# Kernel tuning notes

Hardware: AMD Instinct MI355X
Metric: run time of the kernel (lower is better)

Reference implementation:

```python
import jax, jax.numpy as jnp
import numpy as np

N, E, IN, HID, H, L, G = 20000, 320000, 128, 64, 4, 3, 128

def setup_inputs() -> dict:
    key = jax.random.key(0)
    ks = jax.random.split(key, 14)
    x = jax.random.normal(ks[0], (N, IN), dtype=jnp.float32)
    edge_index = jax.random.randint(ks[1], (2, E), 0, N, dtype=jnp.int64)
    batch = jnp.sort(jax.random.randint(ks[2], (N,), 0, G, dtype=jnp.int64))
    s_in = 1.0 / np.sqrt(IN)
    s_h = 1.0 / np.sqrt(HID)
    lin_W = jax.random.normal(ks[3], (IN, HID), jnp.float32) * s_in
    lin_b = jax.random.normal(ks[4], (HID,), jnp.float32) * 0.02
    Wq = jax.random.normal(ks[5], (L, HID, H * HID), jnp.float32) * s_h
    bq = jax.random.normal(ks[6], (L, H * HID), jnp.float32) * 0.02
    Wk = jax.random.normal(ks[7], (L, HID, H * HID), jnp.float32) * s_h
    bk = jax.random.normal(ks[8], (L, H * HID), jnp.float32) * 0.02
    Wv = jax.random.normal(ks[9], (L, HID, H * HID), jnp.float32) * s_h
    bv = jax.random.normal(ks[10], (L, H * HID), jnp.float32) * 0.02
    Ws = jax.random.normal(ks[11], (L, HID, HID), jnp.float32) * s_h
    bs = jax.random.normal(ks[12], (L, HID), jnp.float32) * 0.02
    return {"x": x, "edge_index": edge_index, "batch": batch,
            "lin_W": lin_W, "lin_b": lin_b, "Wq": Wq, "bq": bq,
            "Wk": Wk, "bk": bk, "Wv": Wv, "bv": bv, "Ws": Ws, "bs": bs}

def _transformer_conv(h, src, dst, Wq, bq, Wk, bk, Wv, bv, Ws, bs):
    # PyG TransformerConv(hid, hid, heads=H, concat=False), beta=False, root_weight=True
    n = h.shape[0]
    C = HID  # per-head dim
    q = (h @ Wq + bq).reshape(n, H, C)
    k = (h @ Wk + bk).reshape(n, H, C)
    v = (h @ Wv + bv).reshape(n, H, C)
    # per-edge attention logits: q_i . k_j / sqrt(C), i=dst (target), j=src
    alpha = jnp.einsum('ehc,ehc->eh', q[dst], k[src]) * (1.0 / np.sqrt(C))  # [E,H]
    # segment softmax over edges grouped by target node
    amax = jax.ops.segment_max(alpha, dst, num_segments=n)  # [N,H]
    amax = jnp.where(jnp.isfinite(amax), amax, 0.0)
    ex = jnp.exp(alpha - amax[dst])
    denom = jax.ops.segment_sum(ex, dst, num_segments=n)
    a = ex / jnp.maximum(denom[dst], 1e-16)  # [E,H]
    msg = a[:, :, None] * v[src]  # [E,H,C]
    agg = jax.ops.segment_sum(msg.reshape(-1, H * C), dst, num_segments=n)
    out = agg.reshape(n, H, C).mean(axis=1)  # concat=False -> head mean
    return out + h @ Ws + bs  # root/skip connection

def reference(x, edge_index, batch, lin_W, lin_b, Wq, bq, Wk, bk, Wv, bv, Ws, bs):
    src, dst = edge_index[0], edge_index[1]
    h = x @ lin_W + lin_b  # [N, HID]; dropout inactive in eval
    for l in range(L):
        h = jax.nn.relu(_transformer_conv(h, src, dst, Wq[l], bq[l], Wk[l], bk[l],
                                          Wv[l], bv[l], Ws[l], bs[l]))
    # global_add_pool: sum node features per graph
    return jax.ops.segment_sum(h, batch, num_segments=G)  # [G, HID]
```

## Files before the change

kernel.cpp:

```cpp
#include <hip/hip_runtime.h>
#include <math.h>

#define N_NODES 20000
#define N_EDGES 320000
#define DIM_IN 128
#define HID 64
#define HEADS 4
#define LAYERS 3
#define GRAPHS 128
#define QSS 320

typedef unsigned short ushort;
typedef ushort ushort8 __attribute__((ext_vector_type(8)));
typedef short short8 __attribute__((ext_vector_type(8)));
typedef float f32x4 __attribute__((ext_vector_type(4)));

__device__ __forceinline__ float bf2f(ushort u) {
    return __uint_as_float(((unsigned int)u) << 16);
}
__device__ __forceinline__ ushort f2bf(float f) {
    unsigned int b = __float_as_uint(f);
    return (ushort)((b + 0x7FFFu + ((b >> 16) & 1u)) >> 16);
}


__global__ void hist_kernel(const int* __restrict__ dst, int* __restrict__ counts, int n) {
    int e = blockIdx.x * 256 + threadIdx.x;
    if (e < n) atomicAdd(&counts[dst[e]], 1);
}

__global__ __launch_bounds__(256) void blocksum_kernel(const int* __restrict__ counts,
                                                       int* __restrict__ bsum, int n) {
    int i = blockIdx.x * 256 + threadIdx.x;
    int v = (i < n) ? counts[i] : 0;
    int lane = threadIdx.x & 63, wave = threadIdx.x >> 6;
#pragma unroll
    for (int off = 32; off >= 1; off >>= 1) v += __shfl_xor(v, off);
    __shared__ int ws[4];
    if (lane == 0) ws[wave] = v;
    __syncthreads();
    if (threadIdx.x == 0) bsum[blockIdx.x] = ws[0] + ws[1] + ws[2] + ws[3];
}

__global__ __launch_bounds__(128) void scanb_kernel(const int* __restrict__ bsum,
                                                    int* __restrict__ bexcl, int nb) {
    int tid = threadIdx.x;
    int v = (tid < nb) ? bsum[tid] : 0;
    int lane = tid & 63, wave = tid >> 6;
    int s = v;
#pragma unroll
    for (int off = 1; off < 64; off <<= 1) {
        int t = __shfl_up(s, off);
        if (lane >= off) s += t;
    }
    __shared__ int w0sum;
    if (tid == 63) w0sum = s;
    __syncthreads();
    int excl = s - v + (wave ? w0sum : 0);
    if (tid < nb) bexcl[tid] = excl;
}

__global__ __launch_bounds__(256) void expand_kernel(const int* __restrict__ counts,
                                                     const int* __restrict__ bexcl,
                                                     int* __restrict__ offs,
                                                     int* __restrict__ cursor, int n) {
    int i = blockIdx.x * 256 + threadIdx.x;
    int v = (i < n) ? counts[i] : 0;
    int lane = threadIdx.x & 63, wave = threadIdx.x >> 6;
    int s = v;
#pragma unroll
    for (int off = 1; off < 64; off <<= 1) {
        int t = __shfl_up(s, off);
        if (lane >= off) s += t;
    }
    __shared__ int wsum[4];
    if (lane == 63) wsum[wave] = s;
    __syncthreads();
    int add = bexcl[blockIdx.x];
    for (int w = 0; w < wave; ++w) add += wsum[w];
    int excl = add + s - v;
    if (i < n) { offs[i] = excl; cursor[i] = excl; }
    if (i == 0) offs[n] = N_EDGES;
}

__global__ void scatter_kernel(const int* __restrict__ src, const int* __restrict__ dst,
                               int* __restrict__ cursor, int* __restrict__ csr, int n) {
    int e = blockIdx.x * 256 + threadIdx.x;
    if (e < n) {
        int d = dst[e];
        int pos = atomicAdd(&cursor[d], 1);
        csr[pos] = src[e];
    }
}


__global__ __launch_bounds__(256) void wcvt_all_kernel(
        const float* __restrict__ Wq, const float* __restrict__ bq,
        const float* __restrict__ Wk, const float* __restrict__ bk,
        const float* __restrict__ Wv, const float* __restrict__ bv,
        const float* __restrict__ Ws, const float* __restrict__ bs,
        const float* __restrict__ linW,
        ushort* __restrict__ Wt3, float* __restrict__ bias3,
        ushort* __restrict__ Wlt) {
    const int PER = 832 * 64;
    int idx = blockIdx.x * 256 + threadIdx.x;
    if (idx < 3 * PER) {
        int l = idx / PER;
        int r = idx - l * PER;
        int j = r >> 6, k = r & 63;
        const float* Wq_l = Wq + (size_t)l * HID * 256;
        const float* Wk_l = Wk + (size_t)l * HID * 256;
        const float* Wv_l = Wv + (size_t)l * HID * 256;
        const float* Ws_l = Ws + (size_t)l * HID * 64;
        float w;
        if (j < 256) {
            w = Wq_l[(size_t)k * 256 + j];
        } else if (j < 768) {
            int pout = j - 256;
            int isv = (pout >> 2) & 1;
            int low2 = pout & 3;
            int g = pout >> 3;
            int srccol = (g >> 4) * 64 + (g & 15) * 4 + low2;
            w = isv ? Wv_l[(size_t)k * 256 + srccol] : Wk_l[(size_t)k * 256 + srccol];
        } else {
            w = Ws_l[(size_t)k * 64 + (j - 768)];
        }
        Wt3[idx] = f2bf(w);
    } else {
        int idx2 = idx - 3 * PER;
        if (idx2 < 64 * DIM_IN) {
            int col = idx2 >> 7, k = idx2 & 127;
            Wlt[idx2] = f2bf(linW[(size_t)k * HID + col]);
        }
    }
    if (idx < 3 * 832) {
        int l = idx / 832, j = idx - l * 832;
        float b;
        if (j < 256) {
            b = bq[l * 256 + j];
        } else if (j < 768) {
            int pout = j - 256;
            int isv = (pout >> 2) & 1;
            int low2 = pout & 3;
            int g = pout >> 3;
            int srccol = (g >> 4) * 64 + (g & 15) * 4 + low2;
            b = isv ? bv[l * 256 + srccol] : bk[l * 256 + srccol];
        } else {
            b = bs[l * 64 + (j - 768)];
        }
        bias3[idx] = b;
    }
}


__global__ __launch_bounds__(256) void lin_kernel(const float* __restrict__ x,
                                                  const ushort* __restrict__ Wlt,
                                                  const float* __restrict__ lb,
                                                  float* __restrict__ h0) {
    int tid = threadIdx.x;
    int w = tid >> 6, l = tid & 63;
    int r0 = blockIdx.x * 64 + w * 16;
    int row = r0 + (l & 15);
    int rowc = (row < N_NODES) ? row : (N_NODES - 1);

    short8 a[4];
#pragma unroll
    for (int kc = 0; kc < 4; ++kc) {
        const float* xp = x + (size_t)rowc * DIM_IN + kc * 32 + (l >> 4) * 8;
        float4 f0 = *(const float4*)xp;
        float4 f1 = *(const float4*)(xp + 4);
        ushort8 u;
        u[0] = f2bf(f0.x); u[1] = f2bf(f0.y); u[2] = f2bf(f0.z); u[3] = f2bf(f0.w);
        u[4] = f2bf(f1.x); u[5] = f2bf(f1.y); u[6] = f2bf(f1.z); u[7] = f2bf(f1.w);
        a[kc] = __builtin_bit_cast(short8, u);
    }

    f32x4 acc[4];
#pragma unroll
    for (int t = 0; t < 4; ++t) acc[t] = (f32x4){0.f, 0.f, 0.f, 0.f};

    const ushort* wb = Wlt + (size_t)(l & 15) * DIM_IN + (l >> 4) * 8;
#pragma unroll
    for (int t = 0; t < 4; ++t) {
#pragma unroll
        for (int kc = 0; kc < 4; ++kc) {
            short8 b = *(const short8*)(wb + (size_t)t * 16 * DIM_IN + kc * 32);
            acc[t] = __builtin_amdgcn_mfma_f32_16x16x32_bf16(a[kc], b, acc[t], 0, 0, 0);
        }
    }

    int rbase = r0 + ((l >> 4) << 2);
#pragma unroll
    for (int t = 0; t < 4; ++t) {
        int col = t * 16 + (l & 15);
        float bias = lb[col];
#pragma unroll
        for (int i = 0; i < 4; ++i) {
            int rr = rbase + i;
            if (rr < N_NODES) h0[(size_t)rr * HID + col] = acc[t][i] + bias;
        }
    }
}


__global__ __launch_bounds__(512) void proj_kernel(const float* __restrict__ h,
                                                   const ushort* __restrict__ Wt,
                                                   const float* __restrict__ bias_cat,
                                                   float* __restrict__ qs,
                                                   ushort* __restrict__ kvpack) {
    int tid = threadIdx.x;
    int w = tid >> 6, l = tid & 63;
    int r0 = blockIdx.x * 32 + (w & 1) * 16;
    int c0 = (w >> 1) * 208;
    int row = r0 + (l & 15);
    int koff = (l >> 4) * 8;

    short8 a[2];
#pragma unroll
    for (int m = 0; m < 2; ++m) {
        const float* hp = h + (size_t)row * HID + m * 32 + koff;
        float4 f0 = *(const float4*)hp;
        float4 f1 = *(const float4*)(hp + 4);
        ushort8 u;
        u[0] = f2bf(f0.x); u[1] = f2bf(f0.y); u[2] = f2bf(f0.z); u[3] = f2bf(f0.w);
        u[4] = f2bf(f1.x); u[5] = f2bf(f1.y); u[6] = f2bf(f1.z); u[7] = f2bf(f1.w);
        a[m] = __builtin_bit_cast(short8, u);
    }

    f32x4 acc[13];
#pragma unroll
    for (int t = 0; t < 13; ++t) acc[t] = (f32x4){0.f, 0.f, 0.f, 0.f};

    const ushort* wb = Wt + ((size_t)(c0 + (l & 15))) * HID + koff;
#pragma unroll
    for (int t = 0; t < 13; ++t) {
        short8 b0 = *(const short8*)(wb + (size_t)t * 16 * HID);
        short8 b1 = *(const short8*)(wb + (size_t)t * 16 * HID + 32);
        acc[t] = __builtin_amdgcn_mfma_f32_16x16x32_bf16(a[0], b0, acc[t], 0, 0, 0);
        acc[t] = __builtin_amdgcn_mfma_f32_16x16x32_bf16(a[1], b1, acc[t], 0, 0, 0);
    }

    int colbase = c0 + (l & 15);
    int rbase = r0 + ((l >> 4) << 2);
#pragma unroll
    for (int t = 0; t < 13; ++t) {
        int j = colbase + t * 16;
        float bias = bias_cat[j];
        if (j < 256) {
#pragma unroll
            for (int i = 0; i < 4; ++i)
                qs[(size_t)(rbase + i) * QSS + j] = acc[t][i] + bias;
        } else if (j < 768) {
            int pout = j - 256;
#pragma unroll
            for (int i = 0; i < 4; ++i)
                kvpack[(size_t)(rbase + i) * 512 + pout] = f2bf(acc[t][i] + bias);
        } else {
#pragma unroll
            for (int i = 0; i < 4; ++i)
                qs[(size_t)(rbase + i) * QSS + 256 + (j - 768)] = acc[t][i] + bias;
        }
    }
}


#define LD1(DST, EI) { int ee = (EI) < e1 ? (EI) : (e1 - 1); DST = kvp[(size_t)csr[ee] * 64 + lane]; }

#define PROC(U, EI) do { \
    float p = q.x * bf2f(U[0]) + q.y * bf2f(U[1]) + q.z * bf2f(U[2]) + q.w * bf2f(U[3]); \
    p += __shfl_xor(p, 1); \
    p += __shfl_xor(p, 2); \
    p += __shfl_xor(p, 4); \
    p += __shfl_xor(p, 8); \
    float alpha = ((EI) < e1) ? p * 0.125f : -INFINITY; \
    if (__any(alpha > m)) { \
        float nm = fmaxf(m, alpha); \
        float sc = __expf(m - nm); \
        l *= sc; acc.x *= sc; acc.y *= sc; acc.z *= sc; acc.w *= sc; \
        m = nm; \
    } \
    float pe = __expf(alpha - m); \
    l += pe; \
    acc.x += pe * bf2f(U[4]); \
    acc.y += pe * bf2f(U[5]); \
    acc.z += pe * bf2f(U[6]); \
    acc.w += pe * bf2f(U[7]); \
} while (0)

__global__ __launch_bounds__(256) void edge_kernel(const float* __restrict__ qs,
                                                   const ushort8* __restrict__ kvp,
                                                   const int* __restrict__ offs,
                                                   const int* __restrict__ csr,
                                                   float* __restrict__ hout) {
    int wave = threadIdx.x >> 6;
    int lane = threadIdx.x & 63;
    int node = blockIdx.x * 4 + wave;
    if (node >= N_NODES) return;
    int hh = lane >> 4;
    int cb = (lane & 15) * 4;

    const float* nb = qs + (size_t)node * QSS;
    float4 q = *(const float4*)(nb + hh * 64 + cb);

    float m = -INFINITY, l = 0.f;
    float4 acc = make_float4(0.f, 0.f, 0.f, 0.f);

    int e0 = offs[node], e1 = offs[node + 1];
    int cnt = e1 - e0;

    if (cnt > 0) {
        ushort8 A0, A1, A2, A3, A4, A5, A6, A7;
        LD1(A0, e0 + 0); LD1(A1, e0 + 1); LD1(A2, e0 + 2); LD1(A3, e0 + 3);
        LD1(A4, e0 + 4); LD1(A5, e0 + 5); LD1(A6, e0 + 6); LD1(A7, e0 + 7);
        for (int base = e0; base < e1; base += 8) {
            ushort8 B0, B1, B2, B3, B4, B5, B6, B7;
            bool more = (base + 8) < e1;
            if (more) {
                LD1(B0, base + 8);  LD1(B1, base + 9);  LD1(B2, base + 10); LD1(B3, base + 11);
                LD1(B4, base + 12); LD1(B5, base + 13); LD1(B6, base + 14); LD1(B7, base + 15);
            }
            PROC(A0, base + 0); PROC(A1, base + 1); PROC(A2, base + 2); PROC(A3, base + 3);
            PROC(A4, base + 4); PROC(A5, base + 5); PROC(A6, base + 6); PROC(A7, base + 7);
            if (more) {
                A0 = B0; A1 = B1; A2 = B2; A3 = B3;
                A4 = B4; A5 = B5; A6 = B6; A7 = B7;
            }
        }
    }

    float inv = (l > 0.f) ? (1.f / l) : 0.f;
    float4 r;
    r.x = acc.x * inv;
    r.y = acc.y * inv;
    r.z = acc.z * inv;
    r.w = acc.w * inv;
    r.x += __shfl_xor(r.x, 16); r.x += __shfl_xor(r.x, 32);
    r.y += __shfl_xor(r.y, 16); r.y += __shfl_xor(r.y, 32);
    r.z += __shfl_xor(r.z, 16); r.z += __shfl_xor(r.z, 32);
    r.w += __shfl_xor(r.w, 16); r.w += __shfl_xor(r.w, 32);

    if (hh == 0) {
        float4 s = *(const float4*)(nb + 256 + cb);
        float4 o;
        o.x = fmaxf(r.x * 0.25f + s.x, 0.f);
        o.y = fmaxf(r.y * 0.25f + s.y, 0.f);
        o.z = fmaxf(r.z * 0.25f + s.z, 0.f);
        o.w = fmaxf(r.w * 0.25f + s.w, 0.f);
        *(float4*)(hout + (size_t)node * HID + cb) = o;
    }
}


__global__ __launch_bounds__(256) void pool_kernel(const float* __restrict__ h,
                                                   const int* __restrict__ batch,
                                                   float* __restrict__ out) {
    int g = blockIdx.x;
    int lo = 0, hi = N_NODES;
    while (lo < hi) { int mid = (lo + hi) >> 1; if (batch[mid] < g) lo = mid + 1; else hi = mid; }
    int start = lo;
    hi = N_NODES;
    while (lo < hi) { int mid = (lo + hi) >> 1; if (batch[mid] < g + 1) lo = mid + 1; else hi = mid; }
    int end = lo;
    int c = threadIdx.x & 63;
    int sub = threadIdx.x >> 6;
    float acc = 0.f;
    for (int i = start + sub; i < end; i += 4) acc += h[(size_t)i * HID + c];
    __shared__ float lds[4][64];
    lds[sub][c] = acc;
    __syncthreads();
    if (sub == 0) out[g * HID + c] = lds[0][c] + lds[1][c] + lds[2][c] + lds[3][c];
}


extern "C" void kernel_launch(void* const* d_in, const int* in_sizes, int n_in,
                              void* d_out, int out_size, void* d_ws, size_t ws_size,
                              hipStream_t stream) {
    const float* x    = (const float*)d_in[0];
    const int*   edge = (const int*)d_in[1];
    const int*   batch= (const int*)d_in[2];
    const float* linW = (const float*)d_in[3];
    const float* linb = (const float*)d_in[4];
    const float* Wq   = (const float*)d_in[5];
    const float* bq   = (const float*)d_in[6];
    const float* Wk   = (const float*)d_in[7];
    const float* bk   = (const float*)d_in[8];
    const float* Wv   = (const float*)d_in[9];
    const float* bv   = (const float*)d_in[10];
    const float* Ws   = (const float*)d_in[11];
    const float* bs   = (const float*)d_in[12];
    float* out = (float*)d_out;

    const int* src = edge;
    const int* dst = edge + N_EDGES;

    float* h0  = (float*)d_ws;
    float* h1  = h0 + (size_t)N_NODES * HID;
    float* qs  = h1 + (size_t)N_NODES * HID;
    ushort* kvpack = (ushort*)(qs + (size_t)N_NODES * QSS);
    int* counts = (int*)(kvpack + (size_t)N_NODES * 512);
    int* offs   = counts + N_NODES;
    int* cursor = offs + N_NODES + 1;
    int* csr    = cursor + N_NODES;
    int* bsum   = csr + N_EDGES;
    int* bexcl  = bsum + 128;
    ushort* Wt3 = (ushort*)(bexcl + 128);
    float* bias3 = (float*)(Wt3 + 3 * 832 * 64);
    ushort* Wlt = (ushort*)(bias3 + 3 * 832);

    const int NB = (N_NODES + 255) / 256;

    hipMemsetAsync(counts, 0, N_NODES * sizeof(int), stream);
    hist_kernel<<<(N_EDGES + 255) / 256, 256, 0, stream>>>(dst, counts, N_EDGES);
    blocksum_kernel<<<NB, 256, 0, stream>>>(counts, bsum, N_NODES);
    scanb_kernel<<<1, 128, 0, stream>>>(bsum, bexcl, NB);
    expand_kernel<<<NB, 256, 0, stream>>>(counts, bexcl, offs, cursor, N_NODES);
    scatter_kernel<<<(N_EDGES + 255) / 256, 256, 0, stream>>>(src, dst, cursor, csr, N_EDGES);

    wcvt_all_kernel<<<(3 * 832 * 64 + 64 * DIM_IN + 255) / 256, 256, 0, stream>>>(
        Wq, bq, Wk, bk, Wv, bv, Ws, bs, linW, Wt3, bias3, Wlt);

    lin_kernel<<<(N_NODES + 63) / 64, 256, 0, stream>>>(x, Wlt, linb, h0);

    float* hc = h0;
    float* hn = h1;
    for (int l = 0; l < LAYERS; ++l) {
        proj_kernel<<<N_NODES / 32, 512, 0, stream>>>(hc,
            Wt3 + (size_t)l * 832 * 64, bias3 + (size_t)l * 832, qs, kvpack);
        edge_kernel<<<N_NODES / 4, 256, 0, stream>>>(qs, (const ushort8*)kvpack, offs, csr, hn);
        float* t = hc; hc = hn; hn = t;
    }

    pool_kernel<<<GRAPHS, 256, 0, stream>>>(hc, batch, out);
}
```

Baseline: 396.5 us.

## Transpose MFMA operands for vectorized stores and simplify edge loop prefetch

After: 406.7 us. 1.03x slower.

```diff
diff --git a/kernel.cpp b/kernel.cpp
--- a/kernel.cpp
+++ b/kernel.cpp
@@ -12,6 +12,7 @@
 
 typedef unsigned short ushort;
 typedef ushort ushort8 __attribute__((ext_vector_type(8)));
+typedef ushort ushort4v __attribute__((ext_vector_type(4)));
 typedef short short8 __attribute__((ext_vector_type(8)));
 typedef float f32x4 __attribute__((ext_vector_type(4)));
 
@@ -185,19 +186,21 @@
 #pragma unroll
         for (int kc = 0; kc < 4; ++kc) {
             short8 b = *(const short8*)(wb + (size_t)t * 16 * DIM_IN + kc * 32);
-            acc[t] = __builtin_amdgcn_mfma_f32_16x16x32_bf16(a[kc], b, acc[t], 0, 0, 0);
-        }
-    }
-
-    int rbase = r0 + ((l >> 4) << 2);
-#pragma unroll
-    for (int t = 0; t < 4; ++t) {
-        int col = t * 16 + (l & 15);
-        float bias = lb[col];
-#pragma unroll
-        for (int i = 0; i < 4; ++i) {
-            int rr = rbase + i;
-            if (rr < N_NODES) h0[(size_t)rr * HID + col] = acc[t][i] + bias;
+            acc[t] = __builtin_amdgcn_mfma_f32_16x16x32_bf16(b, a[kc], acc[t], 0, 0, 0);
+        }
+    }
+
+    if (row < N_NODES) {
+#pragma unroll
+        for (int t = 0; t < 4; ++t) {
+            int j = t * 16 + ((l >> 4) << 2);
+            float4 bias = *(const float4*)(lb + j);
+            float4 o;
+            o.x = acc[t][0] + bias.x;
+            o.y = acc[t][1] + bias.y;
+            o.z = acc[t][2] + bias.z;
+            o.w = acc[t][3] + bias.w;
+            *(float4*)(h0 + (size_t)row * HID + j) = o;
         }
     }
 }
@@ -236,56 +239,32 @@
     for (int t = 0; t < 13; ++t) {
         short8 b0 = *(const short8*)(wb + (size_t)t * 16 * HID);
         short8 b1 = *(const short8*)(wb + (size_t)t * 16 * HID + 32);
-        acc[t] = __builtin_amdgcn_mfma_f32_16x16x32_bf16(a[0], b0, acc[t], 0, 0, 0);
-        acc[t] = __builtin_amdgcn_mfma_f32_16x16x32_bf16(a[1], b1, acc[t], 0, 0, 0);
-    }
-
-    int colbase = c0 + (l & 15);
-    int rbase = r0 + ((l >> 4) << 2);
+        acc[t] = __builtin_amdgcn_mfma_f32_16x16x32_bf16(b0, a[0], acc[t], 0, 0, 0);
+        acc[t] = __builtin_amdgcn_mfma_f32_16x16x32_bf16(b1, a[1], acc[t], 0, 0, 0);
+    }
+
 #pragma unroll
     for (int t = 0; t < 13; ++t) {
-        int j = colbase + t * 16;
-        float bias = bias_cat[j];
+        int j = c0 + t * 16 + ((l >> 4) << 2);
+        float4 bias = *(const float4*)(bias_cat + j);
+        float4 o;
+        o.x = acc[t][0] + bias.x;
+        o.y = acc[t][1] + bias.y;
+        o.z = acc[t][2] + bias.z;
+        o.w = acc[t][3] + bias.w;
         if (j < 256) {
-#pragma unroll
-            for (int i = 0; i < 4; ++i)
-                qs[(size_t)(rbase + i) * QSS + j] = acc[t][i] + bias;
+            *(float4*)(qs + (size_t)row * QSS + j) = o;
         } else if (j < 768) {
             int pout = j - 256;
-#pragma unroll
-            for (int i = 0; i < 4; ++i)
-                kvpack[(size_t)(rbase + i) * 512 + pout] = f2bf(acc[t][i] + bias);
+            ushort4v u4;
+            u4[0] = f2bf(o.x); u4[1] = f2bf(o.y); u4[2] = f2bf(o.z); u4[3] = f2bf(o.w);
+            *(ushort4v*)(kvpack + (size_t)row * 512 + pout) = u4;
         } else {
-#pragma unroll
-            for (int i = 0; i < 4; ++i)
-                qs[(size_t)(rbase + i) * QSS + 256 + (j - 768)] = acc[t][i] + bias;
-        }
-    }
-}
-
-
-#define LD1(DST, EI) { int ee = (EI) < e1 ? (EI) : (e1 - 1); DST = kvp[(size_t)csr[ee] * 64 + lane]; }
-
-#define PROC(U, EI) do { \
-    float p = q.x * bf2f(U[0]) + q.y * bf2f(U[1]) + q.z * bf2f(U[2]) + q.w * bf2f(U[3]); \
-    p += __shfl_xor(p, 1); \
-    p += __shfl_xor(p, 2); \
-    p += __shfl_xor(p, 4); \
-    p += __shfl_xor(p, 8); \
-    float alpha = ((EI) < e1) ? p * 0.125f : -INFINITY; \
-    if (__any(alpha > m)) { \
-        float nm = fmaxf(m, alpha); \
-        float sc = __expf(m - nm); \
-        l *= sc; acc.x *= sc; acc.y *= sc; acc.z *= sc; acc.w *= sc; \
-        m = nm; \
-    } \
-    float pe = __expf(alpha - m); \
-    l += pe; \
-    acc.x += pe * bf2f(U[4]); \
-    acc.y += pe * bf2f(U[5]); \
-    acc.z += pe * bf2f(U[6]); \
-    acc.w += pe * bf2f(U[7]); \
-} while (0)
+            *(float4*)(qs + (size_t)row * QSS + 256 + (j - 768)) = o;
+        }
+    }
+}
+
 
 __global__ __launch_bounds__(256) void edge_kernel(const float* __restrict__ qs,
                                                    const ushort8* __restrict__ kvp,
@@ -302,30 +281,42 @@
     const float* nb = qs + (size_t)node * QSS;
     float4 q = *(const float4*)(nb + hh * 64 + cb);
 
+    const float SCL = 0.125f * 1.44269504088896340736f;
+
     float m = -INFINITY, l = 0.f;
     float4 acc = make_float4(0.f, 0.f, 0.f, 0.f);
 
     int e0 = offs[node], e1 = offs[node + 1];
     int cnt = e1 - e0;
 
-    if (cnt > 0) {
-        ushort8 A0, A1, A2, A3, A4, A5, A6, A7;
-        LD1(A0, e0 + 0); LD1(A1, e0 + 1); LD1(A2, e0 + 2); LD1(A3, e0 + 3);
-        LD1(A4, e0 + 4); LD1(A5, e0 + 5); LD1(A6, e0 + 6); LD1(A7, e0 + 7);
-        for (int base = e0; base < e1; base += 8) {
-            ushort8 B0, B1, B2, B3, B4, B5, B6, B7;
-            bool more = (base + 8) < e1;
-            if (more) {
-                LD1(B0, base + 8);  LD1(B1, base + 9);  LD1(B2, base + 10); LD1(B3, base + 11);
-                LD1(B4, base + 12); LD1(B5, base + 13); LD1(B6, base + 14); LD1(B7, base + 15);
-            }
-            PROC(A0, base + 0); PROC(A1, base + 1); PROC(A2, base + 2); PROC(A3, base + 3);
-            PROC(A4, base + 4); PROC(A5, base + 5); PROC(A6, base + 6); PROC(A7, base + 7);
-            if (more) {
-                A0 = B0; A1 = B1; A2 = B2; A3 = B3;
-                A4 = B4; A5 = B5; A6 = B6; A7 = B7;
-            }
-        }
+    ushort8 cur = (ushort8)(0);
+    ushort8 nxt = (ushort8)(0);
+    if (cnt > 0) cur = kvp[(size_t)csr[e0] * 64 + lane];
+    if (cnt > 1) nxt = kvp[(size_t)csr[e0 + 1] * 64 + lane];
+
+    for (int i = 0; i < cnt; ++i) {
+        ushort8 u = cur;
+        cur = nxt;
+        if (i + 2 < cnt) nxt = kvp[(size_t)csr[e0 + i + 2] * 64 + lane];
+
+        float p = q.x * bf2f(u[0]) + q.y * bf2f(u[1]) + q.z * bf2f(u[2]) + q.w * bf2f(u[3]);
+        p += __shfl_xor(p, 1);
+        p += __shfl_xor(p, 2);
+        p += __shfl_xor(p, 4);
+        p += __shfl_xor(p, 8);
+        float alpha = p * SCL;
+        if (__any(alpha > m)) {
+            float nm = fmaxf(m, alpha);
+            float sc = exp2f(m - nm);
+            l *= sc; acc.x *= sc; acc.y *= sc; acc.z *= sc; acc.w *= sc;
+            m = nm;
+        }
+        float pe = exp2f(alpha - m);
+        l += pe;
+        acc.x += pe * bf2f(u[4]);
+        acc.y += pe * bf2f(u[5]);
+        acc.z += pe * bf2f(u[6]);
+        acc.w += pe * bf2f(u[7]);
     }
 
     float inv = (l > 0.f) ? (1.f / l) : 0.f;
```
